# Optimization experiments

Hardware: AMD Instinct MI355X
Metric: run time of the kernel (lower is better)

Reference implementation:

```python
import jax, jax.numpy as jnp
import numpy as np

GROUP_SIZE = 64
OUT_F, IN_F = 11008, 4096
W_SHAPE = (OUT_F, IN_F)


def quantize_q40(w):
    # w: fp32 weight, numel divisible by GROUP_SIZE
    wg = w.reshape(-1, GROUP_SIZE)                      # [N, G]
    wmax = jnp.max(jnp.abs(wg), axis=1)
    scale = (wmax / 7.0).astype(jnp.float16)[:, None]   # [N, 1] fp16 per-group scale
    quant = wg / scale.astype(jnp.float32)
    q = jnp.round(quant).astype(jnp.int8)               # values in [-7, 7]
    pairs = q.reshape(-1, 2, GROUP_SIZE)                # even rows -> MSB nibble, odd -> LSB
    packed = ((pairs[:, 0] << 4) | (pairs[:, 1] & 15)).astype(jnp.int8)  # [N/2, G]
    return packed, scale


def dequantize_q40(w, scale):
    # w: int8 packed [N/2, G]; arithmetic shifts sign-extend each nibble
    msb = w >> 4
    lsb = (w << 4) >> 4
    full = jnp.concatenate([msb, lsb], axis=1).reshape(-1, GROUP_SIZE)  # interleave back to [N, G]
    return (full.astype(jnp.float16) * scale).reshape(W_SHAPE)


def setup_inputs() -> dict:
    key = jax.random.key(0)
    kx, kw = jax.random.split(key)
    x = jax.random.normal(kx, (4, 2048, IN_F), dtype=jnp.float16)
    w_fp = jax.random.normal(kw, W_SHAPE, dtype=jnp.float32) * 0.02
    linear_w, linear_s = quantize_q40(w_fp)
    return {"x": x, "linear_w": linear_w, "linear_s": linear_s}


def reference(x, linear_w, linear_s):
    # dequantize packed int4 weights to fp16, then dense linear (no bias)
    deq = dequantize_q40(linear_w, linear_s)            # [OUT_F, IN_F] fp16
    return jnp.einsum('bsi,oi->bso', x, deq)            # F.linear(x, deq)
```

## Files before the change

### kernel.cpp

```cpp
#include <hip/hip_runtime.h>
#include <stdint.h>

#define IN_F   4096
#define OUT_F  11008
#define M_ROWS 8192
#define BM 256
#define BN 256
#define BK 32
#define NTILE_K (IN_F / BK)

typedef __attribute__((ext_vector_type(4))) float  f32x4;
typedef __attribute__((ext_vector_type(4))) int    int4v;
typedef __attribute__((ext_vector_type(8))) unsigned short ushort8;
typedef __bf16 bf16x8 __attribute__((ext_vector_type(8)));

__device__ __forceinline__ unsigned short f2bf(float f) {
  unsigned int u = __builtin_bit_cast(unsigned int, f);
  u += 0x7fffu + ((u >> 16) & 1u);
  return (unsigned short)(u >> 16);
}

__global__ __launch_bounds__(256) void dequant_q40(const int* __restrict__ w,
                                                   const float* __restrict__ sc,
                                                   unsigned short* __restrict__ wb) {
  const int total8 = (OUT_F * IN_F) / 8;
  for (int t = blockIdx.x * blockDim.x + threadIdx.x; t < total8;
       t += gridDim.x * blockDim.x) {
    const int f0  = t * 8;
    const int p   = f0 >> 7;
    const int nib = (f0 >> 6) & 1;
    const int j0  = f0 & 63;
    const float scale = sc[f0 >> 6];
    const int* src = w + p * 64 + j0;
    const int4v b0 = *reinterpret_cast<const int4v*>(src);
    const int4v b1 = *reinterpret_cast<const int4v*>(src + 4);
    ushort8 r;
#pragma unroll
    for (int e = 0; e < 4; ++e) {
      const int v0 = b0[e], v1 = b1[e];
      const int q0 = nib ? ((v0 << 28) >> 28) : (v0 >> 4);
      const int q1 = nib ? ((v1 << 28) >> 28) : (v1 >> 4);
      r[e]     = f2bf((float)q0 * scale);
      r[4 + e] = f2bf((float)q1 * scale);
    }
    *reinterpret_cast<ushort8*>(wb + f0) = r;
  }
}

__global__ __launch_bounds__(256) void cvt_x(const float* __restrict__ x,
                                             unsigned short* __restrict__ xb) {
  const int total8 = (M_ROWS * IN_F) / 8;
  for (int t = blockIdx.x * blockDim.x + threadIdx.x; t < total8;
       t += gridDim.x * blockDim.x) {
    const f32x4 a0 = *reinterpret_cast<const f32x4*>(x + t * 8);
    const f32x4 a1 = *reinterpret_cast<const f32x4*>(x + t * 8 + 4);
    ushort8 r;
#pragma unroll
    for (int e = 0; e < 4; ++e) {
      r[e]     = f2bf(a0[e]);
      r[4 + e] = f2bf(a1[e]);
    }
    *reinterpret_cast<ushort8*>(xb + t * 8) = r;
  }
}

__device__ __forceinline__ void gld16(const void* g, void* l) {
  __builtin_amdgcn_global_load_lds(
      (const __attribute__((address_space(1))) unsigned int*)(uintptr_t)g,
      (__attribute__((address_space(3))) unsigned int*)(unsigned int)(uintptr_t)l,
      16, 0, 0);
}

__global__ __launch_bounds__(512, 2) void gemm_bt(const unsigned short* __restrict__ A,
                                                  const unsigned short* __restrict__ B,
                                                  float* __restrict__ C) {
  __shared__ __align__(16) unsigned short lds[49152];

  const int NT  = OUT_F / BN;
  const int nwg = (M_ROWS / BM) * NT;
  const int cpx = nwg >> 3;
  const int bid = blockIdx.x;
  const int swz = (bid & 7) * cpx + (bid >> 3);
  const int mt  = swz / NT;
  const int nt  = swz - mt * NT;

  const int tid  = threadIdx.x;
  const int lane = tid & 63;
  const int wid  = tid >> 6;
  const int wr   = wid >> 2;
  const int wc   = wid & 3;

  const unsigned short* gA = A + (size_t)(mt * BM + (tid >> 2)) * IN_F + (tid & 3) * 8;
  const unsigned short* gB = B + (size_t)(nt * BM + (tid >> 2)) * IN_F + (tid & 3) * 8;
  unsigned short* ldsw = lds + tid * 8;

#define STAGE(bufi, kk) do {                                   \
    unsigned short* d_ = ldsw + (bufi) * 16384;                \
    gld16(gA + (kk), d_);                                      \
    gld16(gA + (size_t)128 * IN_F + (kk), d_ + 4096);          \
    gld16(gB + (kk), d_ + 8192);                               \
    gld16(gB + (size_t)128 * IN_F + (kk), d_ + 12288);         \
  } while (0)

  const int fr = lane & 15;
  const int kq = (lane >> 4) * 8;
#define RDF(base, row) (*reinterpret_cast<const bf16x8*>((base) + (size_t)(row) * 32 + kq))

  f32x4 acc[8][4] = {};

  STAGE(0, 0);
  STAGE(1, BK);
  asm volatile("s_waitcnt vmcnt(4)" ::: "memory");
  __builtin_amdgcn_s_barrier();
  asm volatile("" ::: "memory");

  int bufi = 0;
  for (int t = 0; t < NTILE_K; ++t) {
    if (t + 2 < NTILE_K) {
      const int b2 = bufi >= 1 ? bufi - 1 : bufi + 2;
      STAGE(b2, (t + 2) * BK);
    }

    const unsigned short* bufA = lds + bufi * 16384;
    const unsigned short* bufB = bufA + 8192;

    bf16x8 bfr[4], afr[8];
#pragma unroll
    for (int nn = 0; nn < 4; ++nn) bfr[nn] = RDF(bufB, wc * 64 + nn * 16 + fr);
#pragma unroll
    for (int mm = 0; mm < 8; ++mm) afr[mm] = RDF(bufA, wr * 128 + mm * 16 + fr);

    __builtin_amdgcn_s_setprio(1);
#pragma unroll
    for (int mm = 0; mm < 8; ++mm)
#pragma unroll
      for (int nn = 0; nn < 4; ++nn)
        acc[mm][nn] = __builtin_amdgcn_mfma_f32_16x16x32_bf16(afr[mm], bfr[nn],
                                                              acc[mm][nn], 0, 0, 0);
    __builtin_amdgcn_s_setprio(0);

    if (t + 2 < NTILE_K)
      asm volatile("s_waitcnt vmcnt(4)" ::: "memory");
    else
      asm volatile("s_waitcnt vmcnt(0)" ::: "memory");
    __builtin_amdgcn_s_barrier();
    asm volatile("" ::: "memory");

    bufi = (bufi >= 2) ? 0 : bufi + 1;
  }

  const int col  = nt * BN + wc * 64 + fr;
  const int row0 = mt * BM + wr * 128 + (lane >> 4) * 4;
#pragma unroll
  for (int m = 0; m < 8; ++m) {
#pragma unroll
    for (int n = 0; n < 4; ++n) {
      float* cp = C + (size_t)(row0 + m * 16) * OUT_F + (col + n * 16);
#pragma unroll
      for (int r = 0; r < 4; ++r) cp[(size_t)r * OUT_F] = acc[m][n][r];
    }
  }
}

extern "C" void kernel_launch(void* const* d_in, const int* in_sizes, int n_in,
                              void* d_out, int out_size, void* d_ws, size_t ws_size,
                              hipStream_t stream) {
  const float* x = (const float*)d_in[0];
  const int*   w = (const int*)d_in[1];
  const float* s = (const float*)d_in[2];
  float*     out = (float*)d_out;

  unsigned short* wb = (unsigned short*)d_ws;
  unsigned short* xb = wb + (size_t)OUT_F * IN_F;

  dequant_q40<<<dim3(2048), dim3(256), 0, stream>>>(w, s, wb);
  cvt_x<<<dim3(2048), dim3(256), 0, stream>>>(x, xb);
  gemm_bt<<<dim3((M_ROWS / BM) * (OUT_F / BN)), dim3(512), 0, stream>>>(xb, wb, out);
}
```

Baseline: 830.4 us.

## Restructure GEMM main loop into 8-wave ping-pong pipeline with swizzled LDS

Raises the K tile to 64, split into two 32-wide halves across two LDS buffers (128 KB). The main loop becomes a fine-grained schedule that interleaves half-tile staging, fragment reads and 16-MFMA groups between barriers, in the style of an 8-wave ping-pong. It also XOR-swizzles the LDS column layout to avoid bank conflicts on fragment reads. The aim is better overlap of global loads and LDS reads with MFMA and fewer LDS conflicts, at the cost of more barriers and double the LDS per workgroup, which may cut occupancy from 2 blocks per CU to 1. Loads past the end of K wrap to index 0, so they do redundant work.

```diff
diff --git a/kernel.cpp b/kernel.cpp
--- a/kernel.cpp
+++ b/kernel.cpp
@@ -6,7 +6,7 @@
 #define M_ROWS 8192
 #define BM 256
 #define BN 256
-#define BK 32
+#define BK 64
 #define NTILE_K (IN_F / BK)
 
 typedef __attribute__((ext_vector_type(4))) float  f32x4;
@@ -71,10 +71,13 @@
       16, 0, 0);
 }
 
+#define BAR() do { asm volatile("" ::: "memory"); __builtin_amdgcn_s_barrier(); \
+                   asm volatile("" ::: "memory"); } while (0)
+
 __global__ __launch_bounds__(512, 2) void gemm_bt(const unsigned short* __restrict__ A,
                                                   const unsigned short* __restrict__ B,
                                                   float* __restrict__ C) {
-  __shared__ __align__(16) unsigned short lds[49152];
+  __shared__ __align__(16) unsigned short lds[65536];
 
   const int NT  = OUT_F / BN;
   const int nwg = (M_ROWS / BM) * NT;
@@ -90,63 +93,81 @@
   const int wr   = wid >> 2;
   const int wc   = wid & 3;
 
-  const unsigned short* gA = A + (size_t)(mt * BM + (tid >> 2)) * IN_F + (tid & 3) * 8;
-  const unsigned short* gB = B + (size_t)(nt * BM + (tid >> 2)) * IN_F + (tid & 3) * 8;
+  const int r_st = tid >> 2;
+  const int lc   = (tid & 3) ^ ((tid >> 3) & 3);
+  const unsigned short* gA = A + (size_t)(mt * BM + r_st) * IN_F + lc * 8;
+  const unsigned short* gB = B + (size_t)(nt * BM + r_st) * IN_F + lc * 8;
   unsigned short* ldsw = lds + tid * 8;
 
-#define STAGE(bufi, kk) do {                                   \
-    unsigned short* d_ = ldsw + (bufi) * 16384;                \
-    gld16(gA + (kk), d_);                                      \
-    gld16(gA + (size_t)128 * IN_F + (kk), d_ + 4096);          \
-    gld16(gB + (kk), d_ + 8192);                               \
-    gld16(gB + (size_t)128 * IN_F + (kk), d_ + 12288);         \
-  } while (0)
-
-  const int fr = lane & 15;
-  const int kq = (lane >> 4) * 8;
-#define RDF(base, row) (*reinterpret_cast<const bf16x8*>((base) + (size_t)(row) * 32 + kq))
+#define STAGE_A(b, h, kk) do {                                              \
+    unsigned short* d_ = ldsw + (b) * 32768 + (h) * 8192;                   \
+    const unsigned short* s_ = gA + (kk) + (h) * 32;                        \
+    gld16(s_, d_); gld16(s_ + (size_t)128 * IN_F, d_ + 4096);               \
+  } while (0)
+#define STAGE_B(b, h, kk) do {                                              \
+    unsigned short* d_ = ldsw + (b) * 32768 + 16384 + (h) * 8192;           \
+    const unsigned short* s_ = gB + (kk) + (h) * 32;                        \
+    gld16(s_, d_); gld16(s_ + (size_t)128 * IN_F, d_ + 4096);               \
+  } while (0)
+
+  const int fr   = lane & 15;
+  const int kq   = lane >> 4;
+  const int coff = (kq ^ ((fr >> 1) & 3)) * 8;
+
+  bf16x8 afr[4], bfr[4];
+#define RD_A(b, h, mq) do {                                                 \
+    const unsigned short* p_ = lds + (b) * 32768 + (h) * 8192 + coff;       \
+    _Pragma("unroll") for (int mm = 0; mm < 4; ++mm)                        \
+      afr[mm] = *reinterpret_cast<const bf16x8*>(                           \
+          p_ + (size_t)(wr * 128 + (mq) * 64 + mm * 16 + fr) * 32);         \
+  } while (0)
+#define RD_B(b, h) do {                                                     \
+    const unsigned short* p_ = lds + (b) * 32768 + 16384 + (h) * 8192 + coff; \
+    _Pragma("unroll") for (int nn = 0; nn < 4; ++nn)                        \
+      bfr[nn] = *reinterpret_cast<const bf16x8*>(                           \
+          p_ + (size_t)(wc * 64 + nn * 16 + fr) * 32);                      \
+  } while (0)
 
   f32x4 acc[8][4] = {};
-
-  STAGE(0, 0);
-  STAGE(1, BK);
+#define MFMA16(mq) do {                                                     \
+    __builtin_amdgcn_s_setprio(1);                                          \
+    _Pragma("unroll") for (int mm = 0; mm < 4; ++mm)                        \
+      _Pragma("unroll") for (int nn = 0; nn < 4; ++nn)                      \
+        acc[(mq)*4+mm][nn] = __builtin_amdgcn_mfma_f32_16x16x32_bf16(       \
+            afr[mm], bfr[nn], acc[(mq)*4+mm][nn], 0, 0, 0);                 \
+    __builtin_amdgcn_s_setprio(0);                                          \
+  } while (0)
+
+  STAGE_A(0, 0, 0); STAGE_B(0, 0, 0); STAGE_A(0, 1, 0); STAGE_B(0, 1, 0);
+  STAGE_A(1, 0, BK); STAGE_B(1, 0, BK);
   asm volatile("s_waitcnt vmcnt(4)" ::: "memory");
-  __builtin_amdgcn_s_barrier();
-  asm volatile("" ::: "memory");
-
-  int bufi = 0;
-  for (int t = 0; t < NTILE_K; ++t) {
-    if (t + 2 < NTILE_K) {
-      const int b2 = bufi >= 1 ? bufi - 1 : bufi + 2;
-      STAGE(b2, (t + 2) * BK);
-    }
-
-    const unsigned short* bufA = lds + bufi * 16384;
-    const unsigned short* bufB = bufA + 8192;
-
-    bf16x8 bfr[4], afr[8];
-#pragma unroll
-    for (int nn = 0; nn < 4; ++nn) bfr[nn] = RDF(bufB, wc * 64 + nn * 16 + fr);
-#pragma unroll
-    for (int mm = 0; mm < 8; ++mm) afr[mm] = RDF(bufA, wr * 128 + mm * 16 + fr);
-
-    __builtin_amdgcn_s_setprio(1);
-#pragma unroll
-    for (int mm = 0; mm < 8; ++mm)
-#pragma unroll
-      for (int nn = 0; nn < 4; ++nn)
-        acc[mm][nn] = __builtin_amdgcn_mfma_f32_16x16x32_bf16(afr[mm], bfr[nn],
-                                                              acc[mm][nn], 0, 0, 0);
-    __builtin_amdgcn_s_setprio(0);
-
-    if (t + 2 < NTILE_K)
-      asm volatile("s_waitcnt vmcnt(4)" ::: "memory");
-    else
-      asm volatile("s_waitcnt vmcnt(0)" ::: "memory");
-    __builtin_amdgcn_s_barrier();
-    asm volatile("" ::: "memory");
-
-    bufi = (bufi >= 2) ? 0 : bufi + 1;
+  BAR();
+
+  for (int it = 0; it < NTILE_K / 2; ++it) {
+    const int kt1 = ((2 * it + 1) & (NTILE_K - 1)) * BK;
+    const int kt2 = ((2 * it + 2) & (NTILE_K - 1)) * BK;
+    const int kt3 = ((2 * it + 3) & (NTILE_K - 1)) * BK;
+
+    RD_A(0, 0, 0); RD_B(0, 0); STAGE_A(1, 1, kt1);
+    BAR(); MFMA16(0); BAR();
+    RD_A(0, 0, 1); STAGE_B(1, 1, kt1);
+    BAR(); MFMA16(1); BAR();
+    RD_A(0, 1, 0); RD_B(0, 1); STAGE_A(0, 0, kt2);
+    BAR(); MFMA16(0); BAR();
+    RD_A(0, 1, 1); STAGE_B(0, 0, kt2);
+    BAR(); MFMA16(1);
+    asm volatile("s_waitcnt vmcnt(4)" ::: "memory");
+    BAR();
+    RD_A(1, 0, 0); RD_B(1, 0); STAGE_A(0, 1, kt2);
+    BAR(); MFMA16(0); BAR();
+    RD_A(1, 0, 1); STAGE_B(0, 1, kt2);
+    BAR(); MFMA16(1); BAR();
+    RD_A(1, 1, 0); RD_B(1, 1); STAGE_A(1, 0, kt3);
+    BAR(); MFMA16(0); BAR();
+    RD_A(1, 1, 1); STAGE_B(1, 0, kt3);
+    BAR(); MFMA16(1);
+    asm volatile("s_waitcnt vmcnt(4)" ::: "memory");
+    BAR();
   }
 
   const int col  = nt * BN + wc * 64 + fr;
```

Measured after the change: 775.9 us. -6.6%, faster.
